# Optimization experiments

Measured on AMD Instinct MI355X. Metric: run time of the kernel, lower is better.

## Reference

```python
import jax, jax.numpy as jnp
import numpy as np

B, C_IN, C_OUT, W_DIM = 4, 512, 512, 512
H = W = 84
K = 3
UP = DOWN = 2
TAPS = 12          # filter_size(6) * up_factor(2)
PAD_LO, PAD_HI = 9, 8
SLOPE = 0.2
GAIN = float(np.sqrt(2.0))
CLAMP = 256.0
AFF_GAIN = 1.0 / float(np.sqrt(W_DIM))  # FullyConnectedLayer weight_gain


def _kaiser_beta(a):
    if a > 50:
        return 0.1102 * (a - 8.7)
    if a > 21:
        return 0.5842 * (a - 21.0) ** 0.4 + 0.07886 * (a - 21.0)
    return 0.0


def _design_lowpass(numtaps, cutoff, width, fs):
    # replicates scipy.signal.firwin(numtaps, cutoff, width=width, fs=fs)
    nyq = 0.5 * fs
    atten = 2.285 * (numtaps - 1) * np.pi * (width / nyq) + 7.95
    beta = _kaiser_beta(atten)
    m = np.arange(numtaps) - (numtaps - 1) / 2.0
    c = cutoff / nyq
    h = c * np.sinc(c * m)
    n = np.arange(numtaps)
    win = np.i0(beta * np.sqrt(np.clip(1.0 - (2.0 * n / (numtaps - 1) - 1.0) ** 2, 0.0, 1.0))) / np.i0(beta)
    h = h * win
    h = h / h.sum()
    return jnp.asarray(h, dtype=jnp.float32)


# tmp_sampling_rate = 128; in/out cutoff = 16, half_width = 8 -> width = 16
FU = _design_lowpass(TAPS, 16.0, 16.0, 128.0)
FD = _design_lowpass(TAPS, 16.0, 16.0, 128.0)


def _dwconv(x, f1d, axis, stride=1, dilation=1, pad=(0, 0)):
    # depthwise conv of NCHW x with a 1-D filter along spatial `axis` (2=H, 3=W)
    C = x.shape[1]
    if axis == 2:
        k = jnp.tile(f1d.reshape(1, 1, -1, 1), (C, 1, 1, 1))
        strides, ld, padding = (stride, 1), (dilation, 1), (pad, (0, 0))
    else:
        k = jnp.tile(f1d.reshape(1, 1, 1, -1), (C, 1, 1, 1))
        strides, ld, padding = (1, stride), (1, dilation), ((0, 0), pad)
    return jax.lax.conv_general_dilated(x, k, window_strides=strides, padding=padding,
                                        lhs_dilation=ld,
                                        dimension_numbers=('NCHW', 'OIHW', 'NCHW'),
                                        feature_group_count=C)


def setup_inputs():
    key = jax.random.key(0)
    ks = jax.random.split(key, 5)
    return {
        'x': jax.random.normal(ks[0], (B, C_IN, H, W), jnp.float32),
        'w_latent': jax.random.normal(ks[1], (B, W_DIM), jnp.float32),
        'aff_w': jax.random.normal(ks[2], (C_IN, W_DIM), jnp.float32),
        'aff_b': jnp.ones((C_IN,), jnp.float32),  # bias_init=1
        'conv_w': jax.random.normal(ks[3], (C_OUT, C_IN, K, K), jnp.float32),
        'conv_b': jax.random.normal(ks[4], (C_OUT,), jnp.float32) * 0.1,
    }


def reference(x, w_latent, aff_w, aff_b, conv_w, conv_b):
    # --- style affine (FullyConnectedLayer, linear activation) ---
    s = w_latent @ (aff_w * AFF_GAIN).T + aff_b  # [B, C_IN]
    # --- modulated conv2d with demodulation, folded into input/output scaling ---
    wn = conv_w * jax.lax.rsqrt(jnp.mean(conv_w * conv_w, axis=(1, 2, 3), keepdims=True))
    sn = s * jax.lax.rsqrt(jnp.mean(s * s))
    w2 = jnp.sum(wn * wn, axis=(2, 3))                    # [O, I]
    dcoef = jax.lax.rsqrt((sn * sn) @ w2.T + 1e-8)        # [B, O]
    input_gain = 1.0  # magnitude_ema == 1 -> rsqrt(ema) == 1
    xm = x * (sn * input_gain)[:, :, None, None]
    y = jax.lax.conv_general_dilated(xm, wn, window_strides=(1, 1),
                                     padding=((K - 1, K - 1), (K - 1, K - 1)),
                                     dimension_numbers=('NCHW', 'OIHW', 'NCHW'))
    y = y * dcoef[:, :, None, None]
    # --- filtered leaky-relu: bias -> up-FIR(gain up^2) -> lrelu*sqrt(2), clamp -> FIR-down ---
    y = y + conv_b[None, :, None, None]
    fu = (FU * UP)[::-1]  # total gain up^2 split over the two separable passes; flipped for conv
    y = _dwconv(y, fu, axis=2, dilation=UP, pad=(PAD_LO, PAD_HI + UP - 1))
    y = _dwconv(y, fu, axis=3, dilation=UP, pad=(PAD_LO, PAD_HI + UP - 1))
    y = jnp.where(y < 0, y * SLOPE, y) * GAIN
    y = jnp.clip(y, -CLAMP, CLAMP)
    fd = FD[::-1]
    y = _dwconv(y, fd, axis=2, stride=DOWN)
    y = _dwconv(y, fd, axis=3, stride=DOWN)
    return y  # [B, C_OUT, 84, 84]
```

## Files before the change

kernel.cpp:

```cpp
#include <hip/hip_runtime.h>
#include <hip/hip_bf16.h>
#include <math.h>

typedef __attribute__((ext_vector_type(8))) short bf16x8;
typedef __attribute__((ext_vector_type(4))) float f32x4;

#define B_    4
#define C_    512
#define HW_   84
#define HP_   86
#define XP_   88
#define NPIX  (HP_*HP_)
#define XPIX  (XP_*XP_)
#define YSEG  ((size_t)2048 * NPIX)

struct Taps { float fu[12]; float fd[12]; };

__device__ __forceinline__ unsigned short f2bf(float f) {
    unsigned int u = __float_as_uint(f);
    unsigned int r = (u + 0x7fffu + ((u >> 16) & 1u)) >> 16;
    return (unsigned short)r;
}
__device__ __forceinline__ float bf2f(unsigned short u) {
    return __uint_as_float((unsigned int)u << 16);
}
__device__ __forceinline__ void gload_lds16(const unsigned short* g, unsigned short* l) {
    __builtin_amdgcn_global_load_lds((const __attribute__((address_space(1))) void*)g,
                                     (__attribute__((address_space(3))) void*)l, 16, 0, 0);
}

__global__ __launch_bounds__(256) void k_prep(const float* __restrict__ wlat,
                                              const float* __restrict__ aff_w,
                                              const float* __restrict__ aff_b,
                                              const float* __restrict__ conv_w,
                                              float* __restrict__ s_raw,
                                              float* __restrict__ parts,
                                              unsigned short* __restrict__ wn3,
                                              float* __restrict__ w2) {
    __shared__ float red[256];
    __shared__ float wlds[4608];
    int tid = threadIdx.x;
    if (blockIdx.x < 512) {
        int wv = tid >> 6, lane = tid & 63;
        int w = blockIdx.x * 4 + wv;
        int b = w >> 9, c = w & 511;
        const float4* aw = (const float4*)(aff_w + (size_t)c * 512);
        const float4* wl = (const float4*)(wlat + b * 512);
        float4 a0 = aw[lane * 2], a1 = aw[lane * 2 + 1];
        float4 w0 = wl[lane * 2], w1 = wl[lane * 2 + 1];
        float acc = a0.x * w0.x + a0.y * w0.y + a0.z * w0.z + a0.w * w0.w
                  + a1.x * w1.x + a1.y * w1.y + a1.z * w1.z + a1.w * w1.w;
        #pragma unroll
        for (int m = 1; m < 64; m <<= 1) acc += __shfl_xor(acc, m, 64);
        if (lane == 0) {
            float s = acc * 0.04419417382415922f + aff_b[c];
            s_raw[w] = s; red[wv] = s * s;
        }
        __syncthreads();
        if (tid == 0) parts[blockIdx.x] = red[0] + red[1] + red[2] + red[3];
    } else {
        int o = blockIdx.x - 512;
        const float* wo = conv_w + (size_t)o * 4608;
        float ss = 0.f;
        for (int i = tid; i < 4608; i += 256) { float v = wo[i]; wlds[i] = v; ss += v * v; }
        red[tid] = ss; __syncthreads();
        for (int off = 128; off > 0; off >>= 1) {
            if (tid < off) red[tid] += red[tid + off];
            __syncthreads();
        }
        float scale = rsqrtf(red[0] / 4608.f);
        int og = o >> 5, o32 = o & 31;
        for (int c = tid; c < 512; c += 256) {
            float s2 = 0.f;
            #pragma unroll
            for (int k = 0; k < 9; k++) { float v = wlds[c * 9 + k] * scale; s2 += v * v; }
            w2[(size_t)o * 512 + c] = s2;
        }
        for (int idx = tid; idx < 4608; idx += 256) {
            int cc = idx / 288, rem = idx - cc * 288;
            int kk = rem >> 5, c32 = rem & 31;
            float v = wlds[(cc * 32 + c32) * 9 + kk] * scale;
            wn3[(((size_t)cc * 16 + og) * 32 + o32) * 288 + rem] = f2bf(v);
        }
    }
}

__global__ __launch_bounds__(256) void k_dcoef3(const float* __restrict__ s_raw,
                                                const float* __restrict__ parts,
                                                const float* __restrict__ w2,
                                                float* __restrict__ sn,
                                                float* __restrict__ dcoef) {
    int wv = threadIdx.x >> 6, lane = threadIdx.x & 63;
    int w = blockIdx.x * 4 + wv;
    int b = w >> 9, o = w & 511;
    const float4* pp = (const float4*)parts;
    float4 p0 = pp[lane * 2], p1 = pp[lane * 2 + 1];
    float tot = p0.x + p0.y + p0.z + p0.w + p1.x + p1.y + p1.z + p1.w;
    #pragma unroll
    for (int m = 1; m < 64; m <<= 1) tot += __shfl_xor(tot, m, 64);
    float inv = rsqrtf(tot / 2048.f);
    const float4* sr = (const float4*)(s_raw + b * 512);
    const float4* wr = (const float4*)(w2 + (size_t)o * 512);
    float acc = 0.f;
    #pragma unroll
    for (int q = 0; q < 2; q++) {
        float4 s = sr[lane * 2 + q], ww = wr[lane * 2 + q];
        float s0 = s.x * inv, s1 = s.y * inv, s2 = s.z * inv, s3 = s.w * inv;
        acc += ww.x * s0 * s0 + ww.y * s1 * s1 + ww.z * s2 * s2 + ww.w * s3 * s3;
    }
    #pragma unroll
    for (int m = 1; m < 64; m <<= 1) acc += __shfl_xor(acc, m, 64);
    if (lane == 0) {
        dcoef[w] = rsqrtf(acc + 1e-8f);
        sn[w] = s_raw[w] * inv;
    }
}

__global__ __launch_bounds__(256) void k_premod2(const float* __restrict__ x,
                                                 const float* __restrict__ sn,
                                                 unsigned short* __restrict__ xpad2) {
    int cg = blockIdx.x >> 1, half = blockIdx.x & 1, b = blockIdx.y;
    float sv[8];
    #pragma unroll
    for (int e = 0; e < 8; e++) sv[e] = sn[b * 512 + cg * 8 + e];
    const float* xbase = x + ((size_t)(b * 512 + cg * 8)) * (HW_ * HW_);
    unsigned short* op = xpad2 + ((size_t)(b * 64 + cg)) * XPIX * 8;
    int p0 = half * (XPIX / 2), p1 = p0 + XPIX / 2;
    for (int pix = p0 + threadIdx.x; pix < p1; pix += 256) {
        int r = pix / XP_, cc = pix % XP_;
        unsigned int d[4] = {0u, 0u, 0u, 0u};
        if (r >= 2 && r < 86 && cc >= 2 && cc < 86) {
            int off = (r - 2) * HW_ + (cc - 2);
            #pragma unroll
            for (int e = 0; e < 4; e++) {
                unsigned short lo = f2bf(xbase[(size_t)(2 * e) * (HW_ * HW_) + off] * sv[2 * e]);
                unsigned short hi = f2bf(xbase[(size_t)(2 * e + 1) * (HW_ * HW_) + off] * sv[2 * e + 1]);
                d[e] = (unsigned int)lo | ((unsigned int)hi << 16);
            }
        }
        uint4 v; v.x = d[0]; v.y = d[1]; v.z = d[2]; v.w = d[3];
        *(uint4*)(op + (size_t)pix * 8) = v;
    }
}

__global__ __launch_bounds__(256, 3) void k_conv9(const unsigned short* __restrict__ xpad2,
                                                  const unsigned short* __restrict__ wn3,
                                                  const float* __restrict__ dcoef,
                                                  const float* __restrict__ conv_b,
                                                  unsigned short* __restrict__ ypart) {
    __shared__ __align__(16) unsigned short xs[2][4][384][8];

    int bid = blockIdx.x;
    int wg = (bid & 7) * 264 + (bid >> 3);
    int tile = wg % 66; int rest = wg / 66;
    int ot = rest & 3; int seg = (rest >> 2) & 1; int b = rest >> 3;

    int tid = threadIdx.x;
    int wv = tid >> 6, lane = tid & 63;
    int kgrp = lane >> 4, ln15 = lane & 15;
    int tr = tile / 6, tc = tile % 6;
    int r0 = tr * 8; if (r0 > 78) r0 = 78;
    int c0p = tc * 16; if (c0p > 70) c0p = 70;
    int og = ot * 4 + wv;

    const unsigned short* xseg = xpad2 + ((size_t)(b * 64 + seg * 32 + wv)) * XPIX * 8;
    int pA = lane, pB = 64 + lane, pC = (128 + lane > 179) ? 179 : 128 + lane;
    const unsigned short* gA = xseg + ((size_t)((r0 + pA / 18) * XP_ + c0p + pA % 18)) * 8;
    const unsigned short* gB = xseg + ((size_t)((r0 + pB / 18) * XP_ + c0p + pB % 18)) * 8;
    const unsigned short* gC = xseg + ((size_t)((r0 + pC / 18) * XP_ + c0p + pC % 18)) * 8;
    const size_t cstride = (size_t)4 * XPIX * 8;

    const unsigned short* wb0 = wn3 + (size_t)(seg * 8) * 147456 + ((size_t)(og * 32 + ln15)) * 288 + kgrp * 8;
    const unsigned short* wb1 = wb0 + (size_t)16 * 288;

    f32x4 acc[8][2];
    #pragma unroll
    for (int g = 0; g < 8; g++) { acc[g][0] = (f32x4){0,0,0,0}; acc[g][1] = (f32x4){0,0,0,0}; }

    auto stage2 = [&](int bf) {
        gload_lds16(gA,           &xs[bf][wv][0][0]);
        gload_lds16(gB,           &xs[bf][wv][64][0]);
        gload_lds16(gC,           &xs[bf][wv][128][0]);
        gload_lds16(gA + cstride, &xs[bf][wv][192][0]);
        gload_lds16(gB + cstride, &xs[bf][wv][256][0]);
        gload_lds16(gC + cstride, &xs[bf][wv][320][0]);
        gA += 2 * cstride; gB += 2 * cstride; gC += 2 * cstride;
    };

    stage2(0);
    __syncthreads();

    #pragma unroll 1
    for (int ph = 0; ph < 4; ++ph) {
        int cur = ph & 1;
        if (ph < 3) stage2(cur ^ 1);
        #pragma unroll
        for (int hf = 0; hf < 2; ++hf) {
            int pbase = hf * 192;
            #pragma unroll
            for (int kw = 0; kw < 3; ++kw) {
                bf16x8 F[10];
                #pragma unroll
                for (int r = 0; r < 10; ++r)
                    F[r] = *(const bf16x8*)&xs[cur][kgrp][pbase + r * 18 + ln15 + kw][0];
                #pragma unroll
                for (int kh = 0; kh < 3; ++kh) {
                    int kk = kh * 3 + kw;
                    bf16x8 W0 = *(const bf16x8*)(wb0 + kk * 32);
                    bf16x8 W1 = *(const bf16x8*)(wb1 + kk * 32);
                    #pragma unroll
                    for (int g = 0; g < 8; ++g) {
                        acc[g][0] = __builtin_amdgcn_mfma_f32_16x16x32_bf16(W0, F[g + kh], acc[g][0], 0, 0, 0);
                        acc[g][1] = __builtin_amdgcn_mfma_f32_16x16x32_bf16(W1, F[g + kh], acc[g][1], 0, 0, 0);
                    }
                }
            }
            wb0 += 147456; wb1 += 147456;
        }
        __syncthreads();
    }

    float dcv[2][4], bvs[2][4];
    #pragma unroll
    for (int nt = 0; nt < 2; nt++)
        #pragma unroll
        for (int r = 0; r < 4; r++) {
            int o = og * 32 + nt * 16 + kgrp * 4 + r;
            dcv[nt][r] = dcoef[b * 512 + o];
            bvs[nt][r] = seg ? conv_b[o] : 0.f;
        }
    unsigned short* yp = ypart + (size_t)seg * YSEG;
    int pcol = c0p + ln15;
    #pragma unroll
    for (int g = 0; g < 8; ++g) {
        int prow = r0 + g;
        #pragma unroll
        for (int nt = 0; nt < 2; nt++)
            #pragma unroll
            for (int r = 0; r < 4; r++) {
                int o = og * 32 + nt * 16 + kgrp * 4 + r;
                yp[((size_t)(b * 512 + o)) * NPIX + prow * HP_ + pcol] =
                    f2bf(acc[g][nt][r] * dcv[nt][r] + bvs[nt][r]);
            }
    }
}

__global__ __launch_bounds__(512) void k_resample3(const unsigned short* __restrict__ ypart,
                                                   float* __restrict__ out, Taps taps) {
    __shared__ __align__(16) char smem[23760 + 25344];
    float (*yt)[96]           = (float(*)[96])smem;
    unsigned short (*upF)[180] = (unsigned short(*)[180])smem;
    float (*upR)[96]          = (float(*)[96])(smem + 23760);
    float (*dv)[180]          = (float(*)[180])(smem + 23760);

    int tid = threadIdx.x;
    int ts = blockIdx.x; int o = blockIdx.y; int b = blockIdx.z;
    int tr = ts * 28;
    const unsigned short* y0b = ypart + ((size_t)(b * 512 + o)) * NPIX;
    const unsigned short* y1b = y0b + YSEG;

    for (int idx = tid; idx < 38 * 94; idx += 512) {
        int rr = idx / 94, cc = idx % 94;
        int gr = tr - 4 + rr, gc = cc - 4;
        float v = 0.f;
        if (gr >= 0 && gr < HP_ && gc >= 0 && gc < HP_) {
            int p = gr * HP_ + gc;
            v = bf2f(y0b[p]) + bf2f(y1b[p]);
        }
        yt[rr][cc] = v;
    }
    __syncthreads();
    for (int idx = tid; idx < 33 * 94; idx += 512) {
        int q = idx / 94, cc = idx % 94;
        float aE = 0.f, aO = 0.f;
        #pragma unroll
        for (int u = 0; u < 6; u++) {
            float v = yt[q + u][cc];
            aE += taps.fu[2 * u + 1] * v;
            aO += taps.fu[2 * u] * v;
        }
        upR[2 * q][cc] = aE; upR[2 * q + 1][cc] = aO;
    }
    __syncthreads();
    for (int idx = tid; idx < 66 * 89; idx += 512) {
        int jr = idx / 89, q = idx % 89;
        float aE = 0.f, aO = 0.f;
        #pragma unroll
        for (int u = 0; u < 6; u++) {
            float v = upR[jr][q + u];
            aE += taps.fu[2 * u + 1] * v;
            aO += taps.fu[2 * u] * v;
        }
        aE = (aE < 0.f ? aE * 0.2f : aE) * 1.4142135623730951f;
        aO = (aO < 0.f ? aO * 0.2f : aO) * 1.4142135623730951f;
        aE = fminf(fmaxf(aE, -256.f), 256.f);
        aO = fminf(fmaxf(aO, -256.f), 256.f);
        unsigned int pk = (unsigned int)f2bf(aE) | ((unsigned int)f2bf(aO) << 16);
        *(unsigned int*)&upF[jr][2 * q] = pk;
    }
    __syncthreads();
    for (int idx = tid; idx < 28 * 89; idx += 512) {
        int ii = idx / 89, jp = idx % 89;
        float a0 = 0.f, a1 = 0.f;
        #pragma unroll
        for (int t = 0; t < 12; t++) {
            unsigned int pk = *(const unsigned int*)&upF[2 * ii + t][2 * jp];
            a0 += taps.fd[t] * bf2f((unsigned short)(pk & 0xffffu));
            a1 += taps.fd[t] * bf2f((unsigned short)(pk >> 16));
        }
        *(float2*)&dv[ii][2 * jp] = make_float2(a0, a1);
    }
    __syncthreads();
    for (int idx = tid; idx < 28 * 84; idx += 512) {
        int ii = idx / 84, jo = idx % 84;
        const float2* dp = (const float2*)&dv[ii][2 * jo];
        float a = 0.f;
        #pragma unroll
        for (int t = 0; t < 6; t++) {
            float2 d = dp[t];
            a += taps.fd[2 * t] * d.x + taps.fd[2 * t + 1] * d.y;
        }
        out[((size_t)(b * 512 + o) * 84 + (tr + ii)) * 84 + jo] = a;
    }
}

static double bessel_i0(double x) {
    double s = 1.0, t = 1.0;
    for (int k = 1; k < 60; k++) {
        double u = x / (2.0 * k);
        t *= u * u;
        s += t;
        if (t < 1e-18 * s) break;
    }
    return s;
}

static void design_taps(float* h12) {
    const int N = 12;
    const double cutoff = 16.0, width = 16.0, fs = 128.0;
    double nyq = 0.5 * fs;
    double atten = 2.285 * (N - 1) * M_PI * (width / nyq) + 7.95;
    double beta;
    if (atten > 50.0) beta = 0.1102 * (atten - 8.7);
    else if (atten > 21.0) beta = 0.5842 * pow(atten - 21.0, 0.4) + 0.07886 * (atten - 21.0);
    else beta = 0.0;
    double c = cutoff / nyq;
    double h[12]; double sum = 0.0;
    double ib = bessel_i0(beta);
    for (int n = 0; n < N; n++) {
        double m = n - (N - 1) / 2.0;
        double xx = c * m;
        double sinc = (xx == 0.0) ? 1.0 : sin(M_PI * xx) / (M_PI * xx);
        double t = 2.0 * n / (N - 1) - 1.0;
        double arg = 1.0 - t * t; if (arg < 0.0) arg = 0.0;
        double w = bessel_i0(beta * sqrt(arg)) / ib;
        h[n] = c * sinc * w;
        sum += h[n];
    }
    for (int n = 0; n < N; n++) h12[n] = (float)(h[n] / sum);
}

extern "C" void kernel_launch(void* const* d_in, const int* in_sizes, int n_in,
                              void* d_out, int out_size, void* d_ws, size_t ws_size,
                              hipStream_t stream) {
    const float* x      = (const float*)d_in[0];
    const float* wlat   = (const float*)d_in[1];
    const float* aff_w  = (const float*)d_in[2];
    const float* aff_b  = (const float*)d_in[3];
    const float* conv_w = (const float*)d_in[4];
    const float* conv_b = (const float*)d_in[5];
    float* out = (float*)d_out;

    char* ws = (char*)d_ws;
    float* sn    = (float*)ws;
    float* dcoef = sn + 2048;
    float* w2    = dcoef + 2048;
    unsigned short* wn3   = (unsigned short*)(w2 + 512 * 512);
    unsigned short* xpad2 = wn3 + (size_t)9 * 512 * 512;
    unsigned short* ypart = xpad2 + (size_t)B_ * 64 * XPIX * 8;
    float* s_raw = (float*)ypart;
    float* parts = s_raw + 2048;

    Taps taps;
    float h[12];
    design_taps(h);
    for (int t = 0; t < 12; t++) {
        taps.fu[t] = 2.0f * h[11 - t];
        taps.fd[t] = h[11 - t];
    }

    k_prep   <<<dim3(1024), dim3(256), 0, stream>>>(wlat, aff_w, aff_b, conv_w, s_raw, parts, wn3, w2);
    k_dcoef3 <<<dim3(512), dim3(256), 0, stream>>>(s_raw, parts, w2, sn, dcoef);
    k_premod2<<<dim3(128, 4), dim3(256), 0, stream>>>(x, sn, xpad2);
    k_conv9  <<<dim3(2112), dim3(256), 0, stream>>>(xpad2, wn3, dcoef, conv_b, ypart);
    k_resample3<<<dim3(3, 512, 4), dim3(512), 0, stream>>>(ypart, out, taps);
}
```

Baseline: 272.5 us.

## Merge dcoef and premod kernels; register-block resample FIR passes

Merges the demodulation-coefficient kernel and the input premodulation kernel into one launch. The premod blocks now compute normalized styles inline from s_raw, so the separate sn buffer is gone. The four FIR stages of the resample kernel are register-blocked: each thread loads a sliding window of values once and produces 3-4 outputs, cutting LDS reads, and the final store becomes a float4 write. This raises register pressure in a 512-thread block and adds tail-handling branches.

```diff
diff --git a/kernel.cpp b/kernel.cpp
--- a/kernel.cpp
+++ b/kernel.cpp
@@ -85,61 +85,61 @@
     }
 }
 
-__global__ __launch_bounds__(256) void k_dcoef3(const float* __restrict__ s_raw,
-                                                const float* __restrict__ parts,
-                                                const float* __restrict__ w2,
-                                                float* __restrict__ sn,
-                                                float* __restrict__ dcoef) {
-    int wv = threadIdx.x >> 6, lane = threadIdx.x & 63;
-    int w = blockIdx.x * 4 + wv;
-    int b = w >> 9, o = w & 511;
+__global__ __launch_bounds__(256) void k_moddc(const float* __restrict__ s_raw,
+                                               const float* __restrict__ parts,
+                                               const float* __restrict__ w2,
+                                               const float* __restrict__ x,
+                                               float* __restrict__ dcoef,
+                                               unsigned short* __restrict__ xpad2) {
+    int lane = threadIdx.x & 63;
     const float4* pp = (const float4*)parts;
     float4 p0 = pp[lane * 2], p1 = pp[lane * 2 + 1];
     float tot = p0.x + p0.y + p0.z + p0.w + p1.x + p1.y + p1.z + p1.w;
     #pragma unroll
     for (int m = 1; m < 64; m <<= 1) tot += __shfl_xor(tot, m, 64);
     float inv = rsqrtf(tot / 2048.f);
-    const float4* sr = (const float4*)(s_raw + b * 512);
-    const float4* wr = (const float4*)(w2 + (size_t)o * 512);
-    float acc = 0.f;
-    #pragma unroll
-    for (int q = 0; q < 2; q++) {
-        float4 s = sr[lane * 2 + q], ww = wr[lane * 2 + q];
-        float s0 = s.x * inv, s1 = s.y * inv, s2 = s.z * inv, s3 = s.w * inv;
-        acc += ww.x * s0 * s0 + ww.y * s1 * s1 + ww.z * s2 * s2 + ww.w * s3 * s3;
-    }
-    #pragma unroll
-    for (int m = 1; m < 64; m <<= 1) acc += __shfl_xor(acc, m, 64);
-    if (lane == 0) {
-        dcoef[w] = rsqrtf(acc + 1e-8f);
-        sn[w] = s_raw[w] * inv;
-    }
-}
-
-__global__ __launch_bounds__(256) void k_premod2(const float* __restrict__ x,
-                                                 const float* __restrict__ sn,
-                                                 unsigned short* __restrict__ xpad2) {
-    int cg = blockIdx.x >> 1, half = blockIdx.x & 1, b = blockIdx.y;
-    float sv[8];
-    #pragma unroll
-    for (int e = 0; e < 8; e++) sv[e] = sn[b * 512 + cg * 8 + e];
-    const float* xbase = x + ((size_t)(b * 512 + cg * 8)) * (HW_ * HW_);
-    unsigned short* op = xpad2 + ((size_t)(b * 64 + cg)) * XPIX * 8;
-    int p0 = half * (XPIX / 2), p1 = p0 + XPIX / 2;
-    for (int pix = p0 + threadIdx.x; pix < p1; pix += 256) {
-        int r = pix / XP_, cc = pix % XP_;
-        unsigned int d[4] = {0u, 0u, 0u, 0u};
-        if (r >= 2 && r < 86 && cc >= 2 && cc < 86) {
-            int off = (r - 2) * HW_ + (cc - 2);
-            #pragma unroll
-            for (int e = 0; e < 4; e++) {
-                unsigned short lo = f2bf(xbase[(size_t)(2 * e) * (HW_ * HW_) + off] * sv[2 * e]);
-                unsigned short hi = f2bf(xbase[(size_t)(2 * e + 1) * (HW_ * HW_) + off] * sv[2 * e + 1]);
-                d[e] = (unsigned int)lo | ((unsigned int)hi << 16);
-            }
-        }
-        uint4 v; v.x = d[0]; v.y = d[1]; v.z = d[2]; v.w = d[3];
-        *(uint4*)(op + (size_t)pix * 8) = v;
+
+    if (blockIdx.x >= 512) {
+        int wv = threadIdx.x >> 6;
+        int w = (blockIdx.x - 512) * 4 + wv;
+        int b = w >> 9, o = w & 511;
+        const float4* sr = (const float4*)(s_raw + b * 512);
+        const float4* wr = (const float4*)(w2 + (size_t)o * 512);
+        float acc = 0.f;
+        #pragma unroll
+        for (int q = 0; q < 2; q++) {
+            float4 s = sr[lane * 2 + q], ww = wr[lane * 2 + q];
+            float s0 = s.x * inv, s1 = s.y * inv, s2 = s.z * inv, s3 = s.w * inv;
+            acc += ww.x * s0 * s0 + ww.y * s1 * s1 + ww.z * s2 * s2 + ww.w * s3 * s3;
+        }
+        #pragma unroll
+        for (int m = 1; m < 64; m <<= 1) acc += __shfl_xor(acc, m, 64);
+        if (lane == 0) dcoef[w] = rsqrtf(acc + 1e-8f);
+    } else {
+        int pb = blockIdx.x;
+        int b = pb >> 7; int rem = pb & 127;
+        int cg = rem >> 1, half = rem & 1;
+        float sv[8];
+        #pragma unroll
+        for (int e = 0; e < 8; e++) sv[e] = s_raw[b * 512 + cg * 8 + e] * inv;
+        const float* xbase = x + ((size_t)(b * 512 + cg * 8)) * (HW_ * HW_);
+        unsigned short* op = xpad2 + ((size_t)(b * 64 + cg)) * XPIX * 8;
+        int p0i = half * (XPIX / 2), p1i = p0i + XPIX / 2;
+        for (int pix = p0i + threadIdx.x; pix < p1i; pix += 256) {
+            int r = pix / XP_, cc = pix % XP_;
+            unsigned int d[4] = {0u, 0u, 0u, 0u};
+            if (r >= 2 && r < 86 && cc >= 2 && cc < 86) {
+                int off = (r - 2) * HW_ + (cc - 2);
+                #pragma unroll
+                for (int e = 0; e < 4; e++) {
+                    unsigned short lo = f2bf(xbase[(size_t)(2 * e) * (HW_ * HW_) + off] * sv[2 * e]);
+                    unsigned short hi = f2bf(xbase[(size_t)(2 * e + 1) * (HW_ * HW_) + off] * sv[2 * e + 1]);
+                    d[e] = (unsigned int)lo | ((unsigned int)hi << 16);
+                }
+            }
+            uint4 v; v.x = d[0]; v.y = d[1]; v.z = d[2]; v.w = d[3];
+            *(uint4*)(op + (size_t)pix * 8) = v;
+        }
     }
 }
 
@@ -245,13 +245,13 @@
     }
 }
 
-__global__ __launch_bounds__(512) void k_resample3(const unsigned short* __restrict__ ypart,
+__global__ __launch_bounds__(512) void k_resample4(const unsigned short* __restrict__ ypart,
                                                    float* __restrict__ out, Taps taps) {
     __shared__ __align__(16) char smem[23760 + 25344];
-    float (*yt)[96]           = (float(*)[96])smem;
+    float (*yt)[96]            = (float(*)[96])smem;
     unsigned short (*upF)[180] = (unsigned short(*)[180])smem;
-    float (*upR)[96]          = (float(*)[96])(smem + 23760);
-    float (*dv)[180]          = (float(*)[180])(smem + 23760);
+    float (*upR)[96]           = (float(*)[96])(smem + 23760);
+    float (*dv)[180]           = (float(*)[180])(smem + 23760);
 
     int tid = threadIdx.x;
     int ts = blockIdx.x; int o = blockIdx.y; int b = blockIdx.z;
@@ -270,57 +270,94 @@
         yt[rr][cc] = v;
     }
     __syncthreads();
-    for (int idx = tid; idx < 33 * 94; idx += 512) {
-        int q = idx / 94, cc = idx % 94;
-        float aE = 0.f, aO = 0.f;
-        #pragma unroll
-        for (int u = 0; u < 6; u++) {
-            float v = yt[q + u][cc];
-            aE += taps.fu[2 * u + 1] * v;
-            aO += taps.fu[2 * u] * v;
-        }
-        upR[2 * q][cc] = aE; upR[2 * q + 1][cc] = aO;
+    for (int idx = tid; idx < 11 * 94; idx += 512) {
+        int ri = idx / 94, cc = idx % 94;
+        int q0 = ri * 3;
+        float w[8];
+        #pragma unroll
+        for (int u = 0; u < 8; u++) w[u] = yt[q0 + u][cc];
+        #pragma unroll
+        for (int j = 0; j < 3; j++) {
+            float aE = 0.f, aO = 0.f;
+            #pragma unroll
+            for (int u = 0; u < 6; u++) {
+                float v = w[j + u];
+                aE += taps.fu[2 * u + 1] * v;
+                aO += taps.fu[2 * u] * v;
+            }
+            upR[2 * (q0 + j)][cc] = aE;
+            upR[2 * (q0 + j) + 1][cc] = aO;
+        }
     }
     __syncthreads();
-    for (int idx = tid; idx < 66 * 89; idx += 512) {
-        int jr = idx / 89, q = idx % 89;
-        float aE = 0.f, aO = 0.f;
-        #pragma unroll
-        for (int u = 0; u < 6; u++) {
-            float v = upR[jr][q + u];
-            aE += taps.fu[2 * u + 1] * v;
-            aO += taps.fu[2 * u] * v;
-        }
-        aE = (aE < 0.f ? aE * 0.2f : aE) * 1.4142135623730951f;
-        aO = (aO < 0.f ? aO * 0.2f : aO) * 1.4142135623730951f;
-        aE = fminf(fmaxf(aE, -256.f), 256.f);
-        aO = fminf(fmaxf(aO, -256.f), 256.f);
-        unsigned int pk = (unsigned int)f2bf(aE) | ((unsigned int)f2bf(aO) << 16);
-        *(unsigned int*)&upF[jr][2 * q] = pk;
+    for (int idx = tid; idx < 66 * 23; idx += 512) {
+        int jr = idx / 23, rq = idx % 23;
+        int q0 = rq * 4;
+        int n = 89 - q0; if (n > 4) n = 4;
+        float w[9];
+        #pragma unroll
+        for (int u = 0; u < 9; u++) w[u] = (u < n + 5) ? upR[jr][q0 + u] : 0.f;
+        #pragma unroll
+        for (int j = 0; j < 4; j++) {
+            if (j < n) {
+                float aE = 0.f, aO = 0.f;
+                #pragma unroll
+                for (int u = 0; u < 6; u++) {
+                    float v = w[j + u];
+                    aE += taps.fu[2 * u + 1] * v;
+                    aO += taps.fu[2 * u] * v;
+                }
+                aE = (aE < 0.f ? aE * 0.2f : aE) * 1.4142135623730951f;
+                aO = (aO < 0.f ? aO * 0.2f : aO) * 1.4142135623730951f;
+                aE = fminf(fmaxf(aE, -256.f), 256.f);
+                aO = fminf(fmaxf(aO, -256.f), 256.f);
+                unsigned int pk = (unsigned int)f2bf(aE) | ((unsigned int)f2bf(aO) << 16);
+                *(unsigned int*)&upF[jr][2 * (q0 + j)] = pk;
+            }
+        }
     }
     __syncthreads();
-    for (int idx = tid; idx < 28 * 89; idx += 512) {
-        int ii = idx / 89, jp = idx % 89;
-        float a0 = 0.f, a1 = 0.f;
-        #pragma unroll
-        for (int t = 0; t < 12; t++) {
-            unsigned int pk = *(const unsigned int*)&upF[2 * ii + t][2 * jp];
-            a0 += taps.fd[t] * bf2f((unsigned short)(pk & 0xffffu));
-            a1 += taps.fd[t] * bf2f((unsigned short)(pk >> 16));
-        }
-        *(float2*)&dv[ii][2 * jp] = make_float2(a0, a1);
+    for (int idx = tid; idx < 7 * 89; idx += 512) {
+        int ri = idx / 89, jp = idx % 89;
+        int ii0 = ri * 4;
+        float lo[18], hi[18];
+        #pragma unroll
+        for (int t = 0; t < 18; t++) {
+            unsigned int pk = *(const unsigned int*)&upF[2 * ii0 + t][2 * jp];
+            lo[t] = bf2f((unsigned short)(pk & 0xffffu));
+            hi[t] = bf2f((unsigned short)(pk >> 16));
+        }
+        #pragma unroll
+        for (int j = 0; j < 4; j++) {
+            float a0 = 0.f, a1 = 0.f;
+            #pragma unroll
+            for (int t = 0; t < 12; t++) {
+                a0 += taps.fd[t] * lo[2 * j + t];
+                a1 += taps.fd[t] * hi[2 * j + t];
+            }
+            *(float2*)&dv[ii0 + j][2 * jp] = make_float2(a0, a1);
+        }
     }
     __syncthreads();
-    for (int idx = tid; idx < 28 * 84; idx += 512) {
-        int ii = idx / 84, jo = idx % 84;
-        const float2* dp = (const float2*)&dv[ii][2 * jo];
-        float a = 0.f;
-        #pragma unroll
-        for (int t = 0; t < 6; t++) {
+    for (int idx = tid; idx < 28 * 21; idx += 512) {
+        int ii = idx / 21, rj = idx % 21;
+        int jo0 = rj * 4;
+        float w[18];
+        const float2* dp = (const float2*)&dv[ii][2 * jo0];
+        #pragma unroll
+        for (int t = 0; t < 9; t++) {
             float2 d = dp[t];
-            a += taps.fd[2 * t] * d.x + taps.fd[2 * t + 1] * d.y;
-        }
-        out[((size_t)(b * 512 + o) * 84 + (tr + ii)) * 84 + jo] = a;
+            w[2 * t] = d.x; w[2 * t + 1] = d.y;
+        }
+        float4 res;
+        #pragma unroll
+        for (int j = 0; j < 4; j++) {
+            float a = 0.f;
+            #pragma unroll
+            for (int t = 0; t < 12; t++) a += taps.fd[t] * w[2 * j + t];
+            ((float*)&res)[j] = a;
+        }
+        *(float4*)&out[((size_t)(b * 512 + o) * 84 + (tr + ii)) * 84 + jo0] = res;
     }
 }
 
@@ -372,8 +409,7 @@
     float* out = (float*)d_out;
 
     char* ws = (char*)d_ws;
-    float* sn    = (float*)ws;
-    float* dcoef = sn + 2048;
+    float* dcoef = (float*)ws + 2048;
     float* w2    = dcoef + 2048;
     unsigned short* wn3   = (unsigned short*)(w2 + 512 * 512);
     unsigned short* xpad2 = wn3 + (size_t)9 * 512 * 512;
@@ -390,8 +426,7 @@
     }
 
     k_prep   <<<dim3(1024), dim3(256), 0, stream>>>(wlat, aff_w, aff_b, conv_w, s_raw, parts, wn3, w2);
-    k_dcoef3 <<<dim3(512), dim3(256), 0, stream>>>(s_raw, parts, w2, sn, dcoef);
-    k_premod2<<<dim3(128, 4), dim3(256), 0, stream>>>(x, sn, xpad2);
+    k_moddc  <<<dim3(1024), dim3(256), 0, stream>>>(s_raw, parts, w2, x, dcoef, xpad2);
     k_conv9  <<<dim3(2112), dim3(256), 0, stream>>>(xpad2, wn3, dcoef, conv_b, ypart);
-    k_resample3<<<dim3(3, 512, 4), dim3(512), 0, stream>>>(ypart, out, taps);
-}
+    k_resample4<<<dim3(3, 512, 4), dim3(512), 0, stream>>>(ypart, out, taps);
+}
```

New measurement: 256.1 us. 6.0% less time.
